# Optimization experiments

Hardware: AMD Instinct MI355X
Metric: run time of the kernel (lower is better)

Reference implementation:

```python
import jax, jax.numpy as jnp
import numpy as np

UNITS = 50257
CUTOFF = [2000, 10000, UNITS]  # _cutoff = cutoff + [units]
C = 1024                        # channels (d_model)
N = 4096                        # flattened tokens (batch*seq)
N_TAILS = len(CUTOFF) - 1       # 2
ROOT_OUT = CUTOFF[0] + N_TAILS  # 2002
TAIL_DIMS = [256, 64]           # round(C/4**(i+1)/8)*8


def setup_inputs() -> dict:
    key = jax.random.key(0)
    ks = jax.random.split(key, 7)
    logits = jax.random.normal(ks[0], (N, C), jnp.float32)
    targets = jax.random.randint(ks[1], (N,), 0, UNITS, jnp.int32)
    s = 0.02
    head_kernel = jax.random.normal(ks[2], (C, ROOT_OUT), jnp.float32) * s
    proj0 = jax.random.normal(ks[3], (C, TAIL_DIMS[0]), jnp.float32) * s
    scale0 = jax.random.normal(ks[4], (TAIL_DIMS[0], CUTOFF[1] - CUTOFF[0]), jnp.float32) * s
    proj1 = jax.random.normal(ks[5], (C, TAIL_DIMS[1]), jnp.float32) * s
    scale1 = jax.random.normal(ks[6], (TAIL_DIMS[1], CUTOFF[2] - CUTOFF[1]), jnp.float32) * s
    return {"logits": logits, "targets": targets, "head_kernel": head_kernel,
            "proj0": proj0, "scale0": scale0, "proj1": proj1, "scale1": scale1}


def _sparse_ce(lg, labels):
    # sparse softmax cross entropy, numerically stable (single logsumexp)
    lse = jax.nn.logsumexp(lg, axis=-1)
    picked = jnp.take_along_axis(lg, labels[:, None].astype(jnp.int32), axis=1)[:, 0]
    return lse - picked


def reference(logits, targets, head_kernel, proj0, scale0, proj1, scale1):
    # Faithful jax version of AdaptiveSoftmax._train_loss (return_probs=False,
    # dropout=0, no bias on Denses, loss_reduction=SUM_OVER_BATCH_SIZE i.e. mean).
    # Dynamic boolean gather is replaced by dense compute + masked mean, which
    # yields identical math under jit (mean over the routed subset).
    root_logits = (logits @ head_kernel).astype(jnp.float32)  # [N, ROOT_OUT]
    root_targets = targets
    tails = [(proj0, scale0), (proj1, scale1)]
    losses = []
    for i, (p, s) in enumerate(tails):
        lo, hi = CUTOFF[i], CUTOFF[i + 1]
        m = (targets >= lo) & (targets < hi)
        root_targets = jnp.where(m, CUTOFF[0] + i, root_targets)
        tail_logits = ((logits @ p) @ s).astype(jnp.float32)  # [N, hi-lo]
        tail_tgt = jnp.clip(targets - lo, 0, hi - lo - 1)
        ce = _sparse_ce(tail_logits, tail_tgt)
        mf = m.astype(jnp.float32)
        losses.append(jnp.sum(ce * mf) / jnp.maximum(jnp.sum(mf), 1.0))
    root_loss = jnp.mean(_sparse_ce(root_logits, root_targets))
    all_losses = jnp.stack([root_loss] + losses)
    return jnp.mean(all_losses)
```

## Files before the change

### kernel.cpp

```cpp
#include <hip/hip_runtime.h>
#include <math.h>
#include <stdint.h>

#define NROWS 4096
#define CDIM 1024
#define T0_LO 2000
#define T0_HI 10000
#define T1_LO 10000
#define ROOT_COLS 2002
#define ROOT_PAD 2048
#define T0_COLS 8000
#define T0_PAD 8064
#define T1_COLS 40257
#define T1_PAD 40320
#define HB_STRIDE 320
#define LOG2E 1.44269504088896340736f
#define LN2 0.69314718055994530942f

using short8  = __attribute__((ext_vector_type(8))) short;
using ushort8 = __attribute__((ext_vector_type(8))) unsigned short;
using floatx4 = __attribute__((ext_vector_type(4))) float;

__device__ __forceinline__ unsigned short f2bf(float x) {
  union { float f; unsigned int u; } v; v.f = x;
  unsigned int r = v.u + 0x7fffu + ((v.u >> 16) & 1u);
  return (unsigned short)(r >> 16);
}
__device__ __forceinline__ float bf2f(unsigned short h) {
  union { unsigned int u; float f; } v; v.u = ((unsigned int)h) << 16;
  return v.f;
}
__device__ __forceinline__ floatx4 mfma16(short8 a, short8 b, floatx4 c) {
  return __builtin_amdgcn_mfma_f32_16x16x32_bf16(a, b, c, 0, 0, 0);
}
__device__ __forceinline__ void stage16(const unsigned short* g,
                                        unsigned short* lds_wave_base, int lane) {
#if __has_builtin(__builtin_amdgcn_global_load_lds)
  __builtin_amdgcn_global_load_lds(
      (const __attribute__((address_space(1))) void*)g,
      (__attribute__((address_space(3))) void*)lds_wave_base, 16, 0, 0);
#else
  ((ushort8*)lds_wave_base)[lane] = *(const ushort8*)g;
#endif
}

static constexpr size_t B_HB  = 0;
static constexpr size_t B_LB  = B_HB + 4096ull * 320 * 2;
static constexpr size_t B_WP  = B_LB + 4096ull * 1024 * 2;
static constexpr size_t B_WH  = B_WP + 384ull * 1024 * 2;
static constexpr size_t B_WS0 = B_WH + 2048ull * 1024 * 2;
static constexpr size_t B_WS1 = B_WS0 + 8064ull * 256 * 2;
static constexpr size_t B_S   = B_WS1 + 40320ull * 64 * 2;
static constexpr size_t B_P   = B_S + 3ull * 4096 * 4;
static constexpr size_t B_I0  = B_P + 3ull * 4096 * 4;
static constexpr size_t B_I1  = B_I0 + 4096ull * 4;
static constexpr size_t B_CNT = B_I1 + 4096ull * 4;

__device__ __forceinline__ void transpose_tile(
    const float* __restrict__ W, unsigned short* __restrict__ Wt,
    int K, int N, int Npad, int nx, int rel, float scale,
    float (*tile)[33], int tid) {
  const int n0 = (rel % nx) * 32, k0 = (rel / nx) * 32;
  const int tx = tid & 31, ty = tid >> 5;
  for (int i = 0; i < 32; i += 8) {
    int k = k0 + ty + i, n = n0 + tx;
    tile[ty + i][tx] = (n < N) ? W[(size_t)k * N + n] * scale : 0.f;
  }
  __syncthreads();
  const int nloc = tid >> 3, kg = tid & 7;
  const int n = n0 + nloc;
  if (n < Npad) {
    union { unsigned short v[4]; uint2 u; } x;
#pragma unroll
    for (int j = 0; j < 4; j++) x.v[j] = f2bf(tile[kg * 4 + j][nloc]);
    *(uint2*)&Wt[(size_t)n * K + k0 + kg * 4] = x.u;
  }
}

#define PA_LB_END   2048
#define PA_WP0_END  (PA_LB_END + 256)
#define PA_WP1_END  (PA_WP0_END + 64)
#define PA_ZERO_END (PA_WP1_END + 32)
#define PA_S_END    (PA_ZERO_END + 4)
#define PA_TOTAL    (PA_S_END + 1)

__global__ __launch_bounds__(256) void prep_a_kernel(
    const float* __restrict__ proj0, const float* __restrict__ proj1,
    const float* __restrict__ logits, const int* __restrict__ targets,
    unsigned short* __restrict__ Wp, unsigned short* __restrict__ Lb,
    float* __restrict__ S, int* __restrict__ idx0, int* __restrict__ idx1,
    int* __restrict__ cnt) {
  __shared__ float tile[32][33];
  const int id = blockIdx.x, tid = threadIdx.x;
  if (id < PA_LB_END) {
    size_t base = (size_t)id * 2048 + tid * 8;
    float4 v0 = *(const float4*)(logits + base);
    float4 v1 = *(const float4*)(logits + base + 4);
    ushort8 h;
    h[0] = f2bf(v0.x); h[1] = f2bf(v0.y); h[2] = f2bf(v0.z); h[3] = f2bf(v0.w);
    h[4] = f2bf(v1.x); h[5] = f2bf(v1.y); h[6] = f2bf(v1.z); h[7] = f2bf(v1.w);
    *(ushort8*)(Lb + base) = h;
    return;
  }
  if (id < PA_WP1_END) {
    if (id < PA_WP0_END)
      transpose_tile(proj0, Wp, 1024, 256, 256, 8, id - PA_LB_END, 1.f, tile, tid);
    else
      transpose_tile(proj1, Wp + 256 * 1024, 1024, 64, 64, 2, id - PA_WP0_END,
                     1.f, tile, tid);
    return;
  }
  if (id < PA_ZERO_END) {
    size_t off = (size_t)(id - PA_WP1_END) * 2048 + tid * 8;
    ushort8 z = {0, 0, 0, 0, 0, 0, 0, 0};
    *(ushort8*)(Wp + 320ull * 1024 + off) = z;
    return;
  }
  if (id < PA_S_END) {
    int rel = id - PA_ZERO_END;
    float4 z = make_float4(0.f, 0.f, 0.f, 0.f);
#pragma unroll
    for (int j = 0; j < 3; j++)
      ((float4*)S)[rel * 768 + j * 256 + tid] = z;
    return;
  }
  __shared__ int base2[2];
  if (tid < 2) base2[tid] = 0;
  __syncthreads();
  for (int n = tid; n < NROWS; n += 256) {
    int t = targets[n];
    if (t >= T0_LO && t < T0_HI) idx0[atomicAdd(&base2[0], 1)] = n;
    else if (t >= T1_LO)         idx1[atomicAdd(&base2[1], 1)] = n;
  }
  __syncthreads();
  if (tid < 2) cnt[tid] = base2[tid];
}

template<int CI>
__device__ __forceinline__ void gemm64_kloop(
    unsigned short* A_lds,
    const unsigned short* Arow,
    const unsigned short* const (&Bbase)[CI],
    floatx4 (&acc)[CI][4], int tid) {
  const int lane = tid & 63, w = tid >> 6;
  const int m = lane & 15, quad = lane >> 4, keym = m & 7;
  int goff[4];
#pragma unroll
  for (int it = 0; it < 4; it++) {
    int s = w * 256 + it * 64 + lane;
    int r = s >> 4, p = s & 15;
    int cq = p ^ (r & 7);
    goff[it] = r * CDIM + cq * 8;
  }
#pragma unroll
  for (int it = 0; it < 4; it++)
    stage16(Arow + goff[it], &A_lds[(w * 256 + it * 64) * 8], lane);
  for (int h = 0; h < 8; h++) {
    unsigned short* cur = A_lds + (h & 1) * (64 * 128);
    unsigned short* nxt = A_lds + ((h + 1) & 1) * (64 * 128);
    __syncthreads();
    if (h + 1 < 8) {
#pragma unroll
      for (int it = 0; it < 4; it++)
        stage16(Arow + goff[it] + (h + 1) * 128,
                &nxt[(w * 256 + it * 64) * 8], lane);
    }
    short8 b[CI][4];
#pragma unroll
    for (int ci = 0; ci < CI; ci++)
#pragma unroll
      for (int ks = 0; ks < 4; ks++)
        b[ci][ks] = *(const short8*)(Bbase[ci] + h * 128 + ks * 32);
    short8 areg[4][4];
#pragma unroll
    for (int t = 0; t < 4; t++)
#pragma unroll
      for (int ks = 0; ks < 4; ks++) {
        int ch = ((ks << 2) + quad) ^ keym;
        areg[t][ks] = *(const short8*)&cur[(t * 16 + m) * 128 + (ch << 3)];
      }
#pragma unroll
    for (int ci = 0; ci < CI; ci++)
#pragma unroll
      for (int ks = 0; ks < 4; ks++)
#pragma unroll
        for (int t = 0; t < 4; t++)
          acc[ci][t] = mfma16(areg[t][ks], b[ci][ks], acc[ci][t]);
  }
}

#define K2_HID      320
#define K2_WH_END   (K2_HID + 2048)
#define K2_WS0_END  (K2_WH_END + 2016)
#define K2_TOTAL    (K2_WS0_END + 2520)

__global__ __launch_bounds__(256) void mid_kernel(
    const float* __restrict__ head, const float* __restrict__ scale0,
    const float* __restrict__ scale1,
    const unsigned short* __restrict__ Lb, const unsigned short* __restrict__ Wp,
    unsigned short* __restrict__ Wh, unsigned short* __restrict__ Ws0,
    unsigned short* __restrict__ Ws1, unsigned short* __restrict__ Hb) {
  __shared__ __align__(16) unsigned char smem2[32768];
  const int id = blockIdx.x, tid = threadIdx.x;
  if (id < K2_HID) {
    const int xcd = id & 7, k = id >> 3;
    const int row0 = (xcd * 8 + (k & 7)) * 64;
    const int cg0 = k >> 3;
    unsigned short* A_lds = (unsigned short*)smem2;
    const int lane = tid & 63, w = tid >> 6;
    const int m = lane & 15, quad = lane >> 4;
    const floatx4 zf = {0.f, 0.f, 0.f, 0.f};
    floatx4 acc[1][4];
#pragma unroll
    for (int t = 0; t < 4; t++) acc[0][t] = zf;
    const unsigned short* Bb[1] = {
        Wp + (size_t)(cg0 * 64 + w * 16 + m) * CDIM + quad * 8};
    gemm64_kloop<1>(A_lds, Lb + (size_t)row0 * CDIM, Bb, acc, tid);
    int n = cg0 * 64 + w * 16 + m;
    if (n < HB_STRIDE) {
#pragma unroll
      for (int t = 0; t < 4; t++)
#pragma unroll
        for (int r = 0; r < 4; r++)
          Hb[(size_t)(row0 + t * 16 + quad * 4 + r) * HB_STRIDE + n] =
              f2bf(acc[0][t][r]);
    }
    return;
  }
  const float* W; unsigned short* Wt; int K, N, Npad, nx, rel; float scale;
  int t = id - K2_HID;
  if (t < 2048)      { W = head;   Wt = Wh;  K = 1024; N = ROOT_COLS; Npad = ROOT_PAD; scale = LOG2E; nx = 64;   rel = t; }
  else if (t < 4064) { W = scale0; Wt = Ws0; K = 256;  N = T0_COLS;   Npad = T0_PAD;   scale = LOG2E; nx = 252;  rel = t - 2048; }
  else               { W = scale1; Wt = Ws1; K = 64;   N = T1_COLS;   Npad = T1_PAD;   scale = LOG2E; nx = 1260; rel = t - 4064; }
  transpose_tile(W, Wt, K, N, Npad, nx, rel, scale, (float(*)[33])smem2, tid);
}

#define MG_ROOT 512
#define MG_T1   480
#define MG_T0   2688
#define MG_PICK 1024
#define MG_TOTAL (MG_ROOT + MG_T1 + MG_T0 + MG_PICK)

__device__ __forceinline__ void root_compute(
    const unsigned short* cur, const short8 (&b)[2][2], floatx4 (&acc)[2][8],
    int m, int quad, int keym) {
#pragma unroll
  for (int hf = 0; hf < 2; hf++) {
    short8 areg[4][2];
#pragma unroll
    for (int t = 0; t < 4; t++)
#pragma unroll
      for (int ks = 0; ks < 2; ks++) {
        int ch = ((ks << 2) + quad) ^ keym;
        areg[t][ks] = *(const short8*)&cur[(hf * 64 + t * 16 + m) * 64 + (ch << 3)];
      }
#pragma unroll
    for (int ci = 0; ci < 2; ci++)
#pragma unroll
      for (int ks = 0; ks < 2; ks++)
#pragma unroll
        for (int t = 0; t < 4; t++)
          acc[ci][hf * 4 + t] = mfma16(areg[t][ks], b[ci][ks], acc[ci][hf * 4 + t]);
  }
}

__device__ __forceinline__ void root_stage(
    const unsigned short* Arow, const int (&goff)[4], int koff,
    unsigned short* buf, int w, int lane) {
#pragma unroll
  for (int it = 0; it < 4; it++)
    stage16(Arow + goff[it] + koff, &buf[(it * 256 + w * 64) * 8], lane);
}

__device__ __forceinline__ void root_loadB(
    const unsigned short* const (&Bb)[2], int koff, short8 (&b)[2][2]) {
#pragma unroll
  for (int ci = 0; ci < 2; ci++)
#pragma unroll
    for (int ks = 0; ks < 2; ks++)
      b[ci][ks] = *(const short8*)(Bb[ci] + koff + ks * 32);
}

__device__ __forceinline__ void root_path(
    unsigned char* smem, int bx, int by,
    const unsigned short* __restrict__ Lb,
    const unsigned short* __restrict__ Wh, float* __restrict__ S) {
  unsigned short* bufA = (unsigned short*)smem;
  unsigned short* bufB = bufA + 128 * 64;
  const int tid = threadIdx.x;
  const int row0 = bx * 128;
  const int cg0 = by * 2;
  const int lane = tid & 63, w = tid >> 6;
  const int m = lane & 15, quad = lane >> 4, keym = m & 7;
  const floatx4 zf = {0.f, 0.f, 0.f, 0.f};
  floatx4 acc[2][8];
#pragma unroll
  for (int ci = 0; ci < 2; ci++)
#pragma unroll
    for (int t = 0; t < 8; t++) acc[ci][t] = zf;
  const unsigned short* Bb[2] = {
      Wh + (size_t)((cg0 + 0) * 64 + w * 16 + m) * CDIM + quad * 8,
      Wh + (size_t)((cg0 + 1) * 64 + w * 16 + m) * CDIM + quad * 8};
  const unsigned short* Arow = Lb + (size_t)row0 * CDIM;
  int goff[4];
#pragma unroll
  for (int it = 0; it < 4; it++) {
    int s = it * 256 + w * 64 + lane;
    int r = s >> 3, p = s & 7;
    int cq = p ^ (r & 7);
    goff[it] = r * CDIM + cq * 8;
  }
  short8 b0[2][2], b1[2][2];
  root_stage(Arow, goff, 0, bufA, w, lane);
  root_loadB(Bb, 0, b0);
  for (int hh = 0; hh < 8; hh++) {
    __syncthreads();
    root_stage(Arow, goff, (hh * 2 + 1) * 64, bufB, w, lane);
    root_loadB(Bb, (hh * 2 + 1) * 64, b1);
    root_compute(bufA, b0, acc, m, quad, keym);
    __syncthreads();
    if (hh < 7) {
      root_stage(Arow, goff, (hh * 2 + 2) * 64, bufA, w, lane);
      root_loadB(Bb, (hh * 2 + 2) * 64, b0);
    }
    root_compute(bufB, b1, acc, m, quad, keym);
  }
  __syncthreads();
  float* sums = (float*)smem;
  if (tid < 128) sums[tid] = 0.f;
  __syncthreads();
#pragma unroll
  for (int t = 0; t < 8; t++)
#pragma unroll
    for (int r = 0; r < 4; r++) {
      float e = __builtin_amdgcn_exp2f(acc[0][t][r]) +
                __builtin_amdgcn_exp2f(acc[1][t][r]);
      e += __shfl_xor(e, 1); e += __shfl_xor(e, 2);
      e += __shfl_xor(e, 4); e += __shfl_xor(e, 8);
      if (m == 0)
        atomicAdd(&sums[(t >> 2) * 64 + (t & 3) * 16 + quad * 4 + r], e);
    }
  __syncthreads();
  if (tid < 128) atomicAdd(&S[row0 + tid], sums[tid]);
}

template<int K, int TILES, int MODE>
__device__ __forceinline__ void tail_path(
    unsigned char* smem, int bx, int by,
    const unsigned short* __restrict__ Hb, int acol0,
    const unsigned short* __restrict__ Wt, int ncgpb,
    const int* __restrict__ idx, const int* __restrict__ cnt,
    float* __restrict__ S) {
  constexpr int BM = TILES * 16;
  constexpr int CpR = K / 8;
  constexpr int KS = K / 32;
  unsigned short* A_lds = (unsigned short*)smem;
  int* row_lds = (int*)(smem + (size_t)BM * K * 2);
  float* sum_lds = (float*)(smem + (size_t)BM * K * 2 + BM * 4);
  const int tid = threadIdx.x;
  const int count = cnt[MODE - 1];
  const int row0 = bx * BM;
  if (row0 >= count) return;
  if (tid < BM) {
    int r = row0 + tid;
    row_lds[tid] = (r < count) ? idx[r] : -1;
    sum_lds[tid] = 0.f;
  }
  __syncthreads();
#pragma unroll
  for (int i = 0; i < BM * CpR / 256; i++) {
    int c = tid + 256 * i;
    int rl = c / CpR, cq = c % CpR;
    int row = row_lds[rl];
    ushort8 v = {0, 0, 0, 0, 0, 0, 0, 0};
    if (row >= 0) v = *(const ushort8*)(Hb + (size_t)row * HB_STRIDE + acol0 + cq * 8);
    *(ushort8*)&A_lds[rl * K + ((cq ^ (rl & 7)) << 3)] = v;
  }
  __syncthreads();
  const int lane = tid & 63, w = tid >> 6;
  const int m = lane & 15, quad = lane >> 4, keym = m & 7;
  const floatx4 zf = {0.f, 0.f, 0.f, 0.f};
  short8 areg[TILES][KS];
#pragma unroll
  for (int t = 0; t < TILES; t++)
#pragma unroll
    for (int ks = 0; ks < KS; ks++) {
      int ch = ((ks << 2) + quad) ^ keym;
      areg[t][ks] = *(const short8*)&A_lds[(t * 16 + m) * K + (ch << 3)];
    }
  float runsum[TILES][4];
#pragma unroll
  for (int t = 0; t < TILES; t++)
#pragma unroll
    for (int r = 0; r < 4; r++) runsum[t][r] = 0.f;

  const int cg0 = by * ncgpb;
  const unsigned short* Bp = Wt + (size_t)(cg0 * 64 + w * 16 + m) * K + quad * 8;
  short8 b0[KS], b1[KS];
#pragma unroll
  for (int ks = 0; ks < KS; ks++) b0[ks] = *(const short8*)(Bp + ks * 32);
#pragma unroll
  for (int ks = 0; ks < KS; ks++)
    b1[ks] = *(const short8*)(Bp + (size_t)64 * K + ks * 32);

  for (int cc = 0; cc < ncgpb; cc += 2) {
    floatx4 acc[TILES];
#pragma unroll
    for (int t = 0; t < TILES; t++) acc[t] = zf;
#pragma unroll
    for (int ks = 0; ks < KS; ks++)
#pragma unroll
      for (int t = 0; t < TILES; t++) acc[t] = mfma16(areg[t][ks], b0[ks], acc[t]);
    if (cc + 2 < ncgpb) {
      const unsigned short* p = Bp + (size_t)(cc + 2) * 64 * K;
#pragma unroll
      for (int ks = 0; ks < KS; ks++) b0[ks] = *(const short8*)(p + ks * 32);
    }
#pragma unroll
    for (int t = 0; t < TILES; t++)
#pragma unroll
      for (int r = 0; r < 4; r++)
        runsum[t][r] += __builtin_amdgcn_exp2f(acc[t][r]);

#pragma unroll
    for (int t = 0; t < TILES; t++) acc[t] = zf;
#pragma unroll
    for (int ks = 0; ks < KS; ks++)
#pragma unroll
      for (int t = 0; t < TILES; t++) acc[t] = mfma16(areg[t][ks], b1[ks], acc[t]);
    if (cc + 3 < ncgpb) {
      const unsigned short* p = Bp + (size_t)(cc + 3) * 64 * K;
#pragma unroll
      for (int ks = 0; ks < KS; ks++) b1[ks] = *(const short8*)(p + ks * 32);
    }
#pragma unroll
    for (int t = 0; t < TILES; t++)
#pragma unroll
      for (int r = 0; r < 4; r++)
        runsum[t][r] += __builtin_amdgcn_exp2f(acc[t][r]);
  }

#pragma unroll
  for (int t = 0; t < TILES; t++)
#pragma unroll
    for (int r = 0; r < 4; r++) {
      float e = runsum[t][r];
      e += __shfl_xor(e, 1); e += __shfl_xor(e, 2);
      e += __shfl_xor(e, 4); e += __shfl_xor(e, 8);
      if (m == 0) atomicAdd(&sum_lds[t * 16 + quad * 4 + r], e);
    }
  __syncthreads();
  if (tid < BM) {
    int row = row_lds[tid];
    if (row >= 0) atomicAdd(&S[row], sum_lds[tid]);
  }
}

__device__ __forceinline__ void picked_path(
    int rel, const float* __restrict__ logits, const int* __restrict__ targets,
    const unsigned short* __restrict__ Wh,
    const unsigned short* __restrict__ Ws0,
    const unsigned short* __restrict__ Ws1,
    const unsigned short* __restrict__ Hb, float* __restrict__ P) {
  const int tid = threadIdx.x, lane = tid & 63;
  const int row = rel * 4 + (tid >> 6);
  const int t = targets[row];
  const int tr = (t >= T0_LO && t < T0_HI) ? T0_LO : ((t >= T1_LO) ? T0_LO + 1 : t);
  const float* a = logits + (size_t)row * CDIM + lane * 16;
  const unsigned short* wr = Wh + (size_t)tr * CDIM + lane * 16;
  float acc = 0.f;
#pragma unroll
  for (int q = 0; q < 2; q++) {
    ushort8 wv = *(const ushort8*)(wr + q * 8);
    float4 a0 = ((const float4*)a)[q * 2];
    float4 a1 = ((const float4*)a)[q * 2 + 1];
    acc += a0.x * bf2f(wv[0]) + a0.y * bf2f(wv[1]) + a0.z * bf2f(wv[2]) + a0.w * bf2f(wv[3]);
    acc += a1.x * bf2f(wv[4]) + a1.y * bf2f(wv[5]) + a1.z * bf2f(wv[6]) + a1.w * bf2f(wv[7]);
  }
#pragma unroll
  for (int off = 1; off < 64; off <<= 1) acc += __shfl_xor(acc, off);
  if (lane == 0) P[row] = acc * LN2;
  if (t >= T0_LO) {
    float acc2 = 0.f;
    if (t < T0_HI) {
      const unsigned short* h = Hb + (size_t)row * HB_STRIDE + lane * 4;
      const unsigned short* w2 = Ws0 + (size_t)(t - T0_LO) * 256 + lane * 4;
#pragma unroll
      for (int j = 0; j < 4; j++) acc2 += bf2f(h[j]) * bf2f(w2[j]);
    } else {
      acc2 = bf2f(Hb[(size_t)row * HB_STRIDE + 256 + lane]) *
             bf2f(Ws1[(size_t)(t - T1_LO) * 64 + lane]);
    }
#pragma unroll
    for (int off = 1; off < 64; off <<= 1) acc2 += __shfl_xor(acc2, off);
    if (lane == 0) P[(t < T0_HI ? NROWS : 2 * NROWS) + row] = acc2 * LN2;
  }
}

__global__ __launch_bounds__(256, 2) void mega_kernel(
    const unsigned short* __restrict__ Lb,
    const unsigned short* __restrict__ Wh,
    const unsigned short* __restrict__ Ws0,
    const unsigned short* __restrict__ Ws1,
    const unsigned short* __restrict__ Hb,
    const float* __restrict__ logits, const int* __restrict__ targets,
    const int* __restrict__ idx0, const int* __restrict__ idx1,
    const int* __restrict__ cnt, float* __restrict__ S, float* __restrict__ P) {
  __shared__ __align__(16) unsigned char smem[32768];
  const int bid = blockIdx.x;
  const int xcd = bid & 7, l = bid >> 3;
  int path, k;
  if (l < 576) {
    int g = l / 9, r = l - g * 9;
    if (r == 0)      { path = 0; k = g; }
    else if (r == 1) { if (g < 60) { path = 1; k = g; }
                       else        { path = 2; k = 320 + (g - 60); } }
    else if (r <= 6) { path = 2; k = g * 5 + (r - 2); }
    else             { path = 3; k = g * 2 + (r - 7); }
  } else {
    path = 2; k = 324 + (l - 576);
  }
  if (path == 0) {
    int wk = xcd * 64 + k;
    root_path(smem, wk >> 4, wk & 15, Lb, Wh, S);
  } else if (path == 1) {
    int wk = xcd * 60 + k;
    tail_path<64, 8, 2>(smem, wk & 31, wk >> 5, Hb, 256, Ws1, 42, idx1, cnt,
                        S + 2 * NROWS);
  } else if (path == 2) {
    int wk = xcd * 336 + k;
    tail_path<256, 2, 1>(smem, wk & 127, wk >> 7, Hb, 0, Ws0, 6, idx0, cnt,
                         S + NROWS);
  } else {
    picked_path(xcd * 128 + k, logits, targets, Wh, Ws0, Ws1, Hb, P);
  }
}

__global__ __launch_bounds__(1024) void loss_kernel(
    const int* __restrict__ targets,
    const float* __restrict__ S,
    const float* __restrict__ P,
    float* __restrict__ out) {
  const int tid = threadIdx.x;
  float sr = 0.f, s0 = 0.f, s1 = 0.f, c0 = 0.f, c1 = 0.f;
  for (int n = tid; n < NROWS; n += 1024) {
    int t = targets[n];
    sr += logf(S[n] - 46.f) - P[n];
    if (t >= T0_LO && t < T0_HI) { s0 += logf(S[NROWS + n] - 64.f) - P[NROWS + n]; c0 += 1.f; }
    else if (t >= T1_LO)         { s1 += logf(S[2 * NROWS + n] - 63.f) - P[2 * NROWS + n]; c1 += 1.f; }
  }
  for (int off = 32; off > 0; off >>= 1) {
    sr += __shfl_down(sr, off);
    s0 += __shfl_down(s0, off);
    s1 += __shfl_down(s1, off);
    c0 += __shfl_down(c0, off);
    c1 += __shfl_down(c1, off);
  }
  __shared__ float red[16][5];
  int wv = tid >> 6;
  if ((tid & 63) == 0) { red[wv][0] = sr; red[wv][1] = s0; red[wv][2] = s1; red[wv][3] = c0; red[wv][4] = c1; }
  __syncthreads();
  if (tid == 0) {
    sr = 0.f; s0 = 0.f; s1 = 0.f; c0 = 0.f; c1 = 0.f;
#pragma unroll
    for (int i = 0; i < 16; i++) {
      sr += red[i][0]; s0 += red[i][1]; s1 += red[i][2];
      c0 += red[i][3]; c1 += red[i][4];
    }
    float root_loss = sr / (float)NROWS;
    float l0 = s0 / fmaxf(c0, 1.f);
    float l1 = s1 / fmaxf(c1, 1.f);
    out[0] = (root_loss + l0 + l1) / 3.f;
  }
}

extern "C" void kernel_launch(void* const* d_in, const int* in_sizes, int n_in,
                              void* d_out, int out_size, void* d_ws, size_t ws_size,
                              hipStream_t stream) {
  const float* logits  = (const float*)d_in[0];
  const int*   targets = (const int*)d_in[1];
  const float* head    = (const float*)d_in[2];
  const float* proj0   = (const float*)d_in[3];
  const float* scale0  = (const float*)d_in[4];
  const float* proj1   = (const float*)d_in[5];
  const float* scale1  = (const float*)d_in[6];
  float* out = (float*)d_out;
  char* ws = (char*)d_ws;

  unsigned short* Hb  = (unsigned short*)(ws + B_HB);
  unsigned short* Lb  = (unsigned short*)(ws + B_LB);
  unsigned short* Wp  = (unsigned short*)(ws + B_WP);
  unsigned short* Wh  = (unsigned short*)(ws + B_WH);
  unsigned short* Ws0 = (unsigned short*)(ws + B_WS0);
  unsigned short* Ws1 = (unsigned short*)(ws + B_WS1);
  float* S = (float*)(ws + B_S);
  float* P = (float*)(ws + B_P);
  int* idx0 = (int*)(ws + B_I0);
  int* idx1 = (int*)(ws + B_I1);
  int* cnt  = (int*)(ws + B_CNT);

  prep_a_kernel<<<PA_TOTAL, 256, 0, stream>>>(proj0, proj1, logits, targets,
                                              Wp, Lb, S, idx0, idx1, cnt);
  mid_kernel<<<K2_TOTAL, 256, 0, stream>>>(head, scale0, scale1, Lb, Wp,
                                           Wh, Ws0, Ws1, Hb);
  mega_kernel<<<MG_TOTAL, 256, 0, stream>>>(Lb, Wh, Ws0, Ws1, Hb, logits,
                                            targets, idx0, idx1, cnt, S, P);
  loss_kernel<<<1, 1024, 0, stream>>>(targets, S, P, out);
}
```

Measured before the change: 202.8 us.

## Rework mega-kernel work split: smaller root tiles, persistent tail loops, higher occupancy

Shrinks the root GEMM tile from 128 to 64 rows, which doubles the root block count and halves its LDS and accumulator footprint. The tail paths become grid-stride persistent loops whose work counts follow the runtime routed-row counts, so blocks are no longer launched for empty tiles. The T0 tail now does one 64-column group per work item, and the interleaved block mapping is replaced by contiguous path ranges. LDS shrinks to about 16KB and launch bounds ask for 4 blocks per SM to raise occupancy. In exchange, the smaller tiles reuse less data, and the dynamic loops may leave the load imbalanced.

```diff
diff --git a/kernel.cpp b/kernel.cpp
--- a/kernel.cpp
+++ b/kernel.cpp
@@ -235,44 +235,41 @@
   transpose_tile(W, Wt, K, N, Npad, nx, rel, scale, (float(*)[33])smem2, tid);
 }
 
-#define MG_ROOT 512
-#define MG_T1   480
-#define MG_T0   2688
 #define MG_PICK 1024
-#define MG_TOTAL (MG_ROOT + MG_T1 + MG_T0 + MG_PICK)
-
-__device__ __forceinline__ void root_compute(
-    const unsigned short* cur, const short8 (&b)[2][2], floatx4 (&acc)[2][8],
+#define MG_ROOT 1024
+#define MG_T1   512
+#define MG_T0   1024
+#define MG_TOTAL (MG_PICK + MG_ROOT + MG_T1 + MG_T0)
+
+__device__ __forceinline__ void root_compute64(
+    const unsigned short* cur, const short8 (&b)[2][2], floatx4 (&acc)[2][4],
     int m, int quad, int keym) {
-#pragma unroll
-  for (int hf = 0; hf < 2; hf++) {
-    short8 areg[4][2];
-#pragma unroll
-    for (int t = 0; t < 4; t++)
-#pragma unroll
-      for (int ks = 0; ks < 2; ks++) {
-        int ch = ((ks << 2) + quad) ^ keym;
-        areg[t][ks] = *(const short8*)&cur[(hf * 64 + t * 16 + m) * 64 + (ch << 3)];
-      }
-#pragma unroll
-    for (int ci = 0; ci < 2; ci++)
-#pragma unroll
-      for (int ks = 0; ks < 2; ks++)
-#pragma unroll
-        for (int t = 0; t < 4; t++)
-          acc[ci][hf * 4 + t] = mfma16(areg[t][ks], b[ci][ks], acc[ci][hf * 4 + t]);
-  }
-}
-
-__device__ __forceinline__ void root_stage(
-    const unsigned short* Arow, const int (&goff)[4], int koff,
+  short8 areg[4][2];
+#pragma unroll
+  for (int t = 0; t < 4; t++)
+#pragma unroll
+    for (int ks = 0; ks < 2; ks++) {
+      int ch = ((ks << 2) + quad) ^ keym;
+      areg[t][ks] = *(const short8*)&cur[(t * 16 + m) * 64 + (ch << 3)];
+    }
+#pragma unroll
+  for (int ci = 0; ci < 2; ci++)
+#pragma unroll
+    for (int ks = 0; ks < 2; ks++)
+#pragma unroll
+      for (int t = 0; t < 4; t++)
+        acc[ci][t] = mfma16(areg[t][ks], b[ci][ks], acc[ci][t]);
+}
+
+__device__ __forceinline__ void root_stage64(
+    const unsigned short* Arow, const int (&goff)[2], int koff,
     unsigned short* buf, int w, int lane) {
 #pragma unroll
-  for (int it = 0; it < 4; it++)
+  for (int it = 0; it < 2; it++)
     stage16(Arow + goff[it] + koff, &buf[(it * 256 + w * 64) * 8], lane);
 }
 
-__device__ __forceinline__ void root_loadB(
+__device__ __forceinline__ void root_loadB64(
     const unsigned short* const (&Bb)[2], int koff, short8 (&b)[2][2]) {
 #pragma unroll
   for (int ci = 0; ci < 2; ci++)
@@ -281,178 +278,246 @@
       b[ci][ks] = *(const short8*)(Bb[ci] + koff + ks * 32);
 }
 
-__device__ __forceinline__ void root_path(
+__device__ __forceinline__ void root_path64(
     unsigned char* smem, int bx, int by,
     const unsigned short* __restrict__ Lb,
     const unsigned short* __restrict__ Wh, float* __restrict__ S) {
   unsigned short* bufA = (unsigned short*)smem;
-  unsigned short* bufB = bufA + 128 * 64;
+  unsigned short* bufB = bufA + 64 * 64;
   const int tid = threadIdx.x;
-  const int row0 = bx * 128;
-  const int cg0 = by * 2;
+  const int row0 = bx * 64, cg0 = by * 2;
   const int lane = tid & 63, w = tid >> 6;
   const int m = lane & 15, quad = lane >> 4, keym = m & 7;
   const floatx4 zf = {0.f, 0.f, 0.f, 0.f};
-  floatx4 acc[2][8];
+  floatx4 acc[2][4];
 #pragma unroll
   for (int ci = 0; ci < 2; ci++)
 #pragma unroll
-    for (int t = 0; t < 8; t++) acc[ci][t] = zf;
+    for (int t = 0; t < 4; t++) acc[ci][t] = zf;
   const unsigned short* Bb[2] = {
       Wh + (size_t)((cg0 + 0) * 64 + w * 16 + m) * CDIM + quad * 8,
       Wh + (size_t)((cg0 + 1) * 64 + w * 16 + m) * CDIM + quad * 8};
   const unsigned short* Arow = Lb + (size_t)row0 * CDIM;
-  int goff[4];
-#pragma unroll
-  for (int it = 0; it < 4; it++) {
+  int goff[2];
+#pragma unroll
+  for (int it = 0; it < 2; it++) {
     int s = it * 256 + w * 64 + lane;
     int r = s >> 3, p = s & 7;
     int cq = p ^ (r & 7);
     goff[it] = r * CDIM + cq * 8;
   }
   short8 b0[2][2], b1[2][2];
-  root_stage(Arow, goff, 0, bufA, w, lane);
-  root_loadB(Bb, 0, b0);
+  root_stage64(Arow, goff, 0, bufA, w, lane);
+  root_loadB64(Bb, 0, b0);
   for (int hh = 0; hh < 8; hh++) {
     __syncthreads();
-    root_stage(Arow, goff, (hh * 2 + 1) * 64, bufB, w, lane);
-    root_loadB(Bb, (hh * 2 + 1) * 64, b1);
-    root_compute(bufA, b0, acc, m, quad, keym);
+    root_stage64(Arow, goff, (hh * 2 + 1) * 64, bufB, w, lane);
+    root_loadB64(Bb, (hh * 2 + 1) * 64, b1);
+    root_compute64(bufA, b0, acc, m, quad, keym);
     __syncthreads();
     if (hh < 7) {
-      root_stage(Arow, goff, (hh * 2 + 2) * 64, bufA, w, lane);
-      root_loadB(Bb, (hh * 2 + 2) * 64, b0);
-    }
-    root_compute(bufB, b1, acc, m, quad, keym);
+      root_stage64(Arow, goff, (hh * 2 + 2) * 64, bufA, w, lane);
+      root_loadB64(Bb, (hh * 2 + 2) * 64, b0);
+    }
+    root_compute64(bufB, b1, acc, m, quad, keym);
   }
   __syncthreads();
   float* sums = (float*)smem;
-  if (tid < 128) sums[tid] = 0.f;
+  if (tid < 64) sums[tid] = 0.f;
   __syncthreads();
 #pragma unroll
-  for (int t = 0; t < 8; t++)
+  for (int t = 0; t < 4; t++)
 #pragma unroll
     for (int r = 0; r < 4; r++) {
       float e = __builtin_amdgcn_exp2f(acc[0][t][r]) +
                 __builtin_amdgcn_exp2f(acc[1][t][r]);
       e += __shfl_xor(e, 1); e += __shfl_xor(e, 2);
       e += __shfl_xor(e, 4); e += __shfl_xor(e, 8);
-      if (m == 0)
-        atomicAdd(&sums[(t >> 2) * 64 + (t & 3) * 16 + quad * 4 + r], e);
+      if (m == 0) atomicAdd(&sums[t * 16 + quad * 4 + r], e);
     }
   __syncthreads();
-  if (tid < 128) atomicAdd(&S[row0 + tid], sums[tid]);
-}
-
-template<int K, int TILES, int MODE>
-__device__ __forceinline__ void tail_path(
-    unsigned char* smem, int bx, int by,
-    const unsigned short* __restrict__ Hb, int acol0,
-    const unsigned short* __restrict__ Wt, int ncgpb,
-    const int* __restrict__ idx, const int* __restrict__ cnt,
-    float* __restrict__ S) {
-  constexpr int BM = TILES * 16;
-  constexpr int CpR = K / 8;
-  constexpr int KS = K / 32;
+  if (tid < 64) atomicAdd(&S[row0 + tid], sums[tid]);
+}
+
+__device__ __forceinline__ void t1_loop(
+    unsigned char* smem, int rel, const unsigned short* __restrict__ Hb,
+    const unsigned short* __restrict__ Ws1, const int* __restrict__ idx,
+    const int* __restrict__ cnt, float* __restrict__ S) {
+  constexpr int BM = 64, K = 64, NCG = 42;
   unsigned short* A_lds = (unsigned short*)smem;
-  int* row_lds = (int*)(smem + (size_t)BM * K * 2);
-  float* sum_lds = (float*)(smem + (size_t)BM * K * 2 + BM * 4);
+  int* row_lds = (int*)(smem + BM * K * 2);
+  float* sum_lds = (float*)(smem + BM * K * 2 + BM * 4);
   const int tid = threadIdx.x;
-  const int count = cnt[MODE - 1];
-  const int row0 = bx * BM;
-  if (row0 >= count) return;
-  if (tid < BM) {
-    int r = row0 + tid;
-    row_lds[tid] = (r < count) ? idx[r] : -1;
-    sum_lds[tid] = 0.f;
-  }
-  __syncthreads();
-#pragma unroll
-  for (int i = 0; i < BM * CpR / 256; i++) {
-    int c = tid + 256 * i;
-    int rl = c / CpR, cq = c % CpR;
-    int row = row_lds[rl];
-    ushort8 v = {0, 0, 0, 0, 0, 0, 0, 0};
-    if (row >= 0) v = *(const ushort8*)(Hb + (size_t)row * HB_STRIDE + acol0 + cq * 8);
-    *(ushort8*)&A_lds[rl * K + ((cq ^ (rl & 7)) << 3)] = v;
-  }
-  __syncthreads();
+  const int count = cnt[1];
+  const int nx = (count + 63) >> 6;
+  const int nworks = nx * 15;
   const int lane = tid & 63, w = tid >> 6;
   const int m = lane & 15, quad = lane >> 4, keym = m & 7;
   const floatx4 zf = {0.f, 0.f, 0.f, 0.f};
-  short8 areg[TILES][KS];
-#pragma unroll
-  for (int t = 0; t < TILES; t++)
-#pragma unroll
-    for (int ks = 0; ks < KS; ks++) {
-      int ch = ((ks << 2) + quad) ^ keym;
-      areg[t][ks] = *(const short8*)&A_lds[(t * 16 + m) * K + (ch << 3)];
-    }
-  float runsum[TILES][4];
-#pragma unroll
-  for (int t = 0; t < TILES; t++)
-#pragma unroll
-    for (int r = 0; r < 4; r++) runsum[t][r] = 0.f;
-
-  const int cg0 = by * ncgpb;
-  const unsigned short* Bp = Wt + (size_t)(cg0 * 64 + w * 16 + m) * K + quad * 8;
-  short8 b0[KS], b1[KS];
-#pragma unroll
-  for (int ks = 0; ks < KS; ks++) b0[ks] = *(const short8*)(Bp + ks * 32);
-#pragma unroll
-  for (int ks = 0; ks < KS; ks++)
-    b1[ks] = *(const short8*)(Bp + (size_t)64 * K + ks * 32);
-
-  for (int cc = 0; cc < ncgpb; cc += 2) {
-    floatx4 acc[TILES];
-#pragma unroll
-    for (int t = 0; t < TILES; t++) acc[t] = zf;
-#pragma unroll
-    for (int ks = 0; ks < KS; ks++)
-#pragma unroll
-      for (int t = 0; t < TILES; t++) acc[t] = mfma16(areg[t][ks], b0[ks], acc[t]);
-    if (cc + 2 < ncgpb) {
-      const unsigned short* p = Bp + (size_t)(cc + 2) * 64 * K;
-#pragma unroll
-      for (int ks = 0; ks < KS; ks++) b0[ks] = *(const short8*)(p + ks * 32);
-    }
-#pragma unroll
-    for (int t = 0; t < TILES; t++)
-#pragma unroll
-      for (int r = 0; r < 4; r++)
-        runsum[t][r] += __builtin_amdgcn_exp2f(acc[t][r]);
-
-#pragma unroll
-    for (int t = 0; t < TILES; t++) acc[t] = zf;
-#pragma unroll
-    for (int ks = 0; ks < KS; ks++)
-#pragma unroll
-      for (int t = 0; t < TILES; t++) acc[t] = mfma16(areg[t][ks], b1[ks], acc[t]);
-    if (cc + 3 < ncgpb) {
-      const unsigned short* p = Bp + (size_t)(cc + 3) * 64 * K;
-#pragma unroll
-      for (int ks = 0; ks < KS; ks++) b1[ks] = *(const short8*)(p + ks * 32);
-    }
-#pragma unroll
-    for (int t = 0; t < TILES; t++)
-#pragma unroll
-      for (int r = 0; r < 4; r++)
-        runsum[t][r] += __builtin_amdgcn_exp2f(acc[t][r]);
-  }
-
-#pragma unroll
-  for (int t = 0; t < TILES; t++)
-#pragma unroll
-    for (int r = 0; r < 4; r++) {
-      float e = runsum[t][r];
-      e += __shfl_xor(e, 1); e += __shfl_xor(e, 2);
-      e += __shfl_xor(e, 4); e += __shfl_xor(e, 8);
-      if (m == 0) atomicAdd(&sum_lds[t * 16 + quad * 4 + r], e);
-    }
-  __syncthreads();
-  if (tid < BM) {
-    int row = row_lds[tid];
-    if (row >= 0) atomicAdd(&S[row], sum_lds[tid]);
+  for (int wk = rel; wk < nworks; wk += MG_T1) {
+    const int by = wk / nx, bx = wk - by * nx;
+    __syncthreads();
+    if (tid < BM) {
+      int r = bx * BM + tid;
+      row_lds[tid] = (r < count) ? idx[r] : -1;
+      sum_lds[tid] = 0.f;
+    }
+    __syncthreads();
+#pragma unroll
+    for (int i = 0; i < 2; i++) {
+      int c = tid + 256 * i;
+      int rl = c >> 3, cq = c & 7;
+      int row = row_lds[rl];
+      ushort8 v = {0, 0, 0, 0, 0, 0, 0, 0};
+      if (row >= 0)
+        v = *(const ushort8*)(Hb + (size_t)row * HB_STRIDE + 256 + cq * 8);
+      *(ushort8*)&A_lds[rl * K + ((cq ^ (rl & 7)) << 3)] = v;
+    }
+    __syncthreads();
+    short8 areg[4][2];
+#pragma unroll
+    for (int t = 0; t < 4; t++)
+#pragma unroll
+      for (int ks = 0; ks < 2; ks++) {
+        int ch = ((ks << 2) + quad) ^ keym;
+        areg[t][ks] = *(const short8*)&A_lds[(t * 16 + m) * K + (ch << 3)];
+      }
+    float runsum[4][4];
+#pragma unroll
+    for (int t = 0; t < 4; t++)
+#pragma unroll
+      for (int r = 0; r < 4; r++) runsum[t][r] = 0.f;
+    const unsigned short* Bp =
+        Ws1 + (size_t)(by * NCG * 64 + w * 16 + m) * K + quad * 8;
+    short8 b0[2], b1[2];
+#pragma unroll
+    for (int ks = 0; ks < 2; ks++) b0[ks] = *(const short8*)(Bp + ks * 32);
+#pragma unroll
+    for (int ks = 0; ks < 2; ks++)
+      b1[ks] = *(const short8*)(Bp + (size_t)64 * K + ks * 32);
+    for (int cc = 0; cc < NCG; cc += 2) {
+      floatx4 acc[4];
+#pragma unroll
+      for (int t = 0; t < 4; t++) acc[t] = zf;
+#pragma unroll
+      for (int ks = 0; ks < 2; ks++)
+#pragma unroll
+        for (int t = 0; t < 4; t++) acc[t] = mfma16(areg[t][ks], b0[ks], acc[t]);
+      if (cc + 2 < NCG) {
+        const unsigned short* p = Bp + (size_t)(cc + 2) * 64 * K;
+#pragma unroll
+        for (int ks = 0; ks < 2; ks++) b0[ks] = *(const short8*)(p + ks * 32);
+      }
+#pragma unroll
+      for (int t = 0; t < 4; t++)
+#pragma unroll
+        for (int r = 0; r < 4; r++)
+          runsum[t][r] += __builtin_amdgcn_exp2f(acc[t][r]);
+#pragma unroll
+      for (int t = 0; t < 4; t++) acc[t] = zf;
+#pragma unroll
+      for (int ks = 0; ks < 2; ks++)
+#pragma unroll
+        for (int t = 0; t < 4; t++) acc[t] = mfma16(areg[t][ks], b1[ks], acc[t]);
+      if (cc + 3 < NCG) {
+        const unsigned short* p = Bp + (size_t)(cc + 3) * 64 * K;
+#pragma unroll
+        for (int ks = 0; ks < 2; ks++) b1[ks] = *(const short8*)(p + ks * 32);
+      }
+#pragma unroll
+      for (int t = 0; t < 4; t++)
+#pragma unroll
+        for (int r = 0; r < 4; r++)
+          runsum[t][r] += __builtin_amdgcn_exp2f(acc[t][r]);
+    }
+#pragma unroll
+    for (int t = 0; t < 4; t++)
+#pragma unroll
+      for (int r = 0; r < 4; r++) {
+        float e = runsum[t][r];
+        e += __shfl_xor(e, 1); e += __shfl_xor(e, 2);
+        e += __shfl_xor(e, 4); e += __shfl_xor(e, 8);
+        if (m == 0) atomicAdd(&sum_lds[t * 16 + quad * 4 + r], e);
+      }
+    __syncthreads();
+    if (tid < BM) {
+      int row = row_lds[tid];
+      if (row >= 0) atomicAdd(&S[2 * NROWS + row], sum_lds[tid]);
+    }
+  }
+}
+
+__device__ __forceinline__ void t0_loop(
+    unsigned char* smem, int rel, const unsigned short* __restrict__ Hb,
+    const unsigned short* __restrict__ Ws0, const int* __restrict__ idx,
+    const int* __restrict__ cnt, float* __restrict__ S) {
+  constexpr int BM = 32, K = 256;
+  unsigned short* A_lds = (unsigned short*)smem;
+  int* row_lds = (int*)(smem + BM * K * 2);
+  float* sum_lds = (float*)(smem + BM * K * 2 + BM * 4);
+  const int tid = threadIdx.x;
+  const int count = cnt[0];
+  const int nx = (count + 31) >> 5;
+  const int nworks = nx * 126;
+  const int lane = tid & 63, w = tid >> 6;
+  const int m = lane & 15, quad = lane >> 4, keym = m & 7;
+  const floatx4 zf = {0.f, 0.f, 0.f, 0.f};
+  for (int wk = rel; wk < nworks; wk += MG_T0) {
+    const int by = wk / nx, bx = wk - by * nx;
+    __syncthreads();
+    if (tid < BM) {
+      int r = bx * BM + tid;
+      row_lds[tid] = (r < count) ? idx[r] : -1;
+      sum_lds[tid] = 0.f;
+    }
+    __syncthreads();
+#pragma unroll
+    for (int i = 0; i < 4; i++) {
+      int c = tid + 256 * i;
+      int rl = c >> 5, cq = c & 31;
+      int row = row_lds[rl];
+      ushort8 v = {0, 0, 0, 0, 0, 0, 0, 0};
+      if (row >= 0)
+        v = *(const ushort8*)(Hb + (size_t)row * HB_STRIDE + cq * 8);
+      *(ushort8*)&A_lds[rl * K + ((cq ^ (rl & 7)) << 3)] = v;
+    }
+    __syncthreads();
+    const unsigned short* Bp =
+        Ws0 + (size_t)(by * 64 + w * 16 + m) * K + quad * 8;
+    floatx4 acc[2] = {zf, zf};
+#pragma unroll
+    for (int half = 0; half < 2; half++) {
+      short8 b[4], areg[2][4];
+#pragma unroll
+      for (int ks = 0; ks < 4; ks++)
+        b[ks] = *(const short8*)(Bp + half * 128 + ks * 32);
+#pragma unroll
+      for (int t = 0; t < 2; t++)
+#pragma unroll
+        for (int ks = 0; ks < 4; ks++) {
+          int ch = (((half * 4 + ks) << 2) + quad) ^ keym;
+          areg[t][ks] = *(const short8*)&A_lds[(t * 16 + m) * K + (ch << 3)];
+        }
+#pragma unroll
+      for (int ks = 0; ks < 4; ks++)
+#pragma unroll
+        for (int t = 0; t < 2; t++)
+          acc[t] = mfma16(areg[t][ks], b[ks], acc[t]);
+    }
+#pragma unroll
+    for (int t = 0; t < 2; t++)
+#pragma unroll
+      for (int r = 0; r < 4; r++) {
+        float e = __builtin_amdgcn_exp2f(acc[t][r]);
+        e += __shfl_xor(e, 1); e += __shfl_xor(e, 2);
+        e += __shfl_xor(e, 4); e += __shfl_xor(e, 8);
+        if (m == 0) atomicAdd(&sum_lds[t * 16 + quad * 4 + r], e);
+      }
+    __syncthreads();
+    if (tid < BM) {
+      int row = row_lds[tid];
+      if (row >= 0) atomicAdd(&S[NROWS + row], sum_lds[tid]);
+    }
   }
 }
 
@@ -497,7 +562,7 @@
   }
 }
 
-__global__ __launch_bounds__(256, 2) void mega_kernel(
+__global__ __launch_bounds__(256, 4) void mega_kernel(
     const unsigned short* __restrict__ Lb,
     const unsigned short* __restrict__ Wh,
     const unsigned short* __restrict__ Ws0,
@@ -506,34 +571,26 @@
     const float* __restrict__ logits, const int* __restrict__ targets,
     const int* __restrict__ idx0, const int* __restrict__ idx1,
     const int* __restrict__ cnt, float* __restrict__ S, float* __restrict__ P) {
-  __shared__ __align__(16) unsigned char smem[32768];
-  const int bid = blockIdx.x;
-  const int xcd = bid & 7, l = bid >> 3;
-  int path, k;
-  if (l < 576) {
-    int g = l / 9, r = l - g * 9;
-    if (r == 0)      { path = 0; k = g; }
-    else if (r == 1) { if (g < 60) { path = 1; k = g; }
-                       else        { path = 2; k = 320 + (g - 60); } }
-    else if (r <= 6) { path = 2; k = g * 5 + (r - 2); }
-    else             { path = 3; k = g * 2 + (r - 7); }
-  } else {
-    path = 2; k = 324 + (l - 576);
-  }
-  if (path == 0) {
-    int wk = xcd * 64 + k;
-    root_path(smem, wk >> 4, wk & 15, Lb, Wh, S);
-  } else if (path == 1) {
-    int wk = xcd * 60 + k;
-    tail_path<64, 8, 2>(smem, wk & 31, wk >> 5, Hb, 256, Ws1, 42, idx1, cnt,
-                        S + 2 * NROWS);
-  } else if (path == 2) {
-    int wk = xcd * 336 + k;
-    tail_path<256, 2, 1>(smem, wk & 127, wk >> 7, Hb, 0, Ws0, 6, idx0, cnt,
-                         S + NROWS);
-  } else {
-    picked_path(xcd * 128 + k, logits, targets, Wh, Ws0, Ws1, Hb, P);
-  }
+  __shared__ __align__(16) unsigned char smem[16640];
+  int bid = blockIdx.x;
+  if (bid < MG_PICK) {
+    picked_path((bid & 7) * 128 + (bid >> 3), logits, targets, Wh, Ws0, Ws1,
+                Hb, P);
+    return;
+  }
+  bid -= MG_PICK;
+  if (bid < MG_ROOT) {
+    const int xcd = bid & 7, j = bid >> 3;
+    root_path64(smem, xcd * 8 + (j & 7), j >> 3, Lb, Wh, S);
+    return;
+  }
+  bid -= MG_ROOT;
+  if (bid < MG_T1) {
+    t1_loop(smem, bid, Hb, Ws1, idx1, cnt, S);
+    return;
+  }
+  bid -= MG_T1;
+  t0_loop(smem, bid, Hb, Ws0, idx0, cnt, S);
 }
 
 __global__ __launch_bounds__(1024) void loss_kernel(
```

Result: faster. 197.0 us (-2.9%).
